# Performance work log

Measured on AMD Instinct MI355X. Metric: run time of the kernel, lower is better.

Reference implementation:

```python
import jax, jax.numpy as jnp
import numpy as np

TEMPERATURE = 0.07
BASE_TEMPERATURE = 0.07
EPI = 0.1
NUM_CLASSES = 100


def setup_inputs() -> dict:
    key = jax.random.key(0)
    k1, k2 = jax.random.split(key)
    bsz, n_views, d = 4096, 2, 256
    features = jax.random.normal(k1, (bsz, n_views, d), dtype=jnp.float32)
    # SupCon features are typically L2-normalized projections
    features = features / jnp.linalg.norm(features, axis=-1, keepdims=True)
    labels = jax.random.randint(k2, (bsz,), 0, NUM_CLASSES, dtype=jnp.int64)
    return {"features": features, "labels": labels}


def reference(features, labels):
    bsz, n_views, d = features.shape
    n = bsz * n_views
    # contrast_feature = cat(unbind(features, dim=1), dim=0): view-major ordering
    contrast = jnp.reshape(jnp.swapaxes(features, 0, 1), (n, d))  # [N, D]
    anchor = contrast  # contrast_mode == 'all'

    labels_t = jnp.tile(labels, n_views)  # [N], matches mask.repeat(anchor_count, contrast_count)
    mask_full = (labels_t[:, None] == labels_t[None, :]).astype(features.dtype)  # [N, N]

    # adversarial similarity: a_i . (c_j - epi * mask_ij * a_i) / T
    sq = jnp.sum(anchor * anchor, axis=1, keepdims=True)  # [N, 1]
    logits_raw = (jnp.matmul(anchor, contrast.T) - EPI * mask_full * sq) / TEMPERATURE

    logits_max = jax.lax.stop_gradient(jnp.max(logits_raw, axis=1, keepdims=True))
    logits = logits_raw - logits_max

    logits_mask = 1.0 - jnp.eye(n, dtype=features.dtype)  # mask out self-contrast
    mask = mask_full * logits_mask

    exp_logits = jnp.exp(logits) * logits_mask
    log_prob = logits - jnp.log(jnp.sum(exp_logits, axis=1, keepdims=True))
    mean_log_prob_pos = jnp.sum(mask * log_prob, axis=1) / jnp.sum(mask, axis=1)

    loss = -(TEMPERATURE / BASE_TEMPERATURE) * mean_log_prob_pos
    return jnp.mean(jnp.reshape(loss, (n_views, bsz)))
```

## Files before the change

### kernel.cpp

```cpp
#include <hip/hip_runtime.h>
#include <hip/hip_bf16.h>

#define NTOT 8192
#define NBSZ 4096
#define DDIM 256
#define NCHUNK 16
#define CHUNK_COLS 512
#define TILE_COLS 32
#define NT (CHUNK_COLS / TILE_COLS)
#define NCLASS 100

#define INV_T 14.285714285714286f
#define EPI_T 1.4285714285714286f
#define K1 20.609929155556076f
#define BIASS -2.0609929155556078f

typedef __attribute__((ext_vector_type(8))) __bf16 bf16x8;
typedef __attribute__((ext_vector_type(4))) float f32x4;

__device__ __forceinline__ unsigned short f2bf(float x) {
    union { float f; unsigned int u; } a; a.f = x;
    unsigned int r = a.u + 0x7fffu + ((a.u >> 16) & 1u);
    return (unsigned short)(r >> 16);
}

__global__ __launch_bounds__(256) void prep_kernel(const float* __restrict__ feat,
                                                   const int* __restrict__ labels,
                                                   unsigned short* __restrict__ Bg,
                                                   int* __restrict__ labT) {
    const int g = blockIdx.x * 256 + threadIdx.x;
    const int row = g >> 6, t = g & 63;
    const int v = row >> 12, b = row & (NBSZ - 1);
    const float* src = feat + (size_t)(b * 2 + v) * DDIM + t * 4;
    f32x4 val = *(const f32x4*)src;
    ushort4 o;
    o.x = f2bf(val[0]); o.y = f2bf(val[1]); o.z = f2bf(val[2]); o.w = f2bf(val[3]);
    *(ushort4*)(Bg + (size_t)row * DDIM + t * 4) = o;
    if (t == 0) labT[row] = labels[b];
}

__device__ __forceinline__ void stage_tile(const unsigned short* __restrict__ Bg,
                                           unsigned short* buf, int colBase, int tid) {
    #pragma unroll
    for (int it = 0; it < 4; ++it) {
        int c = it * 256 + tid;
        int brow = c >> 5, bc = c & 31;
        int sc = bc ^ (brow & 7);
        const unsigned short* src = Bg + (size_t)(colBase + brow) * DDIM + sc * 8;
        __builtin_amdgcn_global_load_lds(
            (const __attribute__((address_space(1))) void*)src,
            (__attribute__((address_space(3))) void*)(buf + (size_t)c * 8),
            16, 0, 0);
    }
}

__global__ __launch_bounds__(256, 2) void supcon_main(
    const unsigned short* __restrict__ Bg, const int* __restrict__ labT,
    float* __restrict__ pSe, float* __restrict__ pPd)
{
    __shared__ alignas(16) unsigned short btile[2][TILE_COLS * DDIM];
    __shared__ int labc_s[CHUNK_COLS];

    const int tid = threadIdx.x;
    const int wid = tid >> 6;
    const int lane = tid & 63;
    const int q = lane >> 4;
    const int r16 = lane & 15;

    const int rowBase = blockIdx.x * 256 + wid * 64;
    const int colChunk = blockIdx.y * CHUNK_COLS;

    labc_s[tid] = labT[colChunk + tid];
    labc_s[tid + 256] = labT[colChunk + 256 + tid];

    bf16x8 afr[4][8];
    #pragma unroll
    for (int m = 0; m < 4; ++m) {
        const unsigned short* ap = Bg + (size_t)(rowBase + m * 16 + r16) * DDIM + q * 8;
        #pragma unroll
        for (int ks = 0; ks < 8; ++ks)
            afr[m][ks] = *(const bf16x8*)(ap + ks * 32);
    }
    int labrow[4][4];
    #pragma unroll
    for (int m = 0; m < 4; ++m)
        #pragma unroll
        for (int r = 0; r < 4; ++r)
            labrow[m][r] = labT[rowBase + m * 16 + q * 4 + r];

    float se[4][4], pd[4][4];
    #pragma unroll
    for (int m = 0; m < 4; ++m)
        #pragma unroll
        for (int r = 0; r < 4; ++r) { se[m][r] = 0.f; pd[m][r] = 0.f; }

    stage_tile(Bg, btile[0], colChunk, tid);
    __syncthreads();

    for (int tile = 0; tile < NT; ++tile) {
        if (tile + 1 < NT)
            stage_tile(Bg, btile[(tile + 1) & 1], colChunk + (tile + 1) * TILE_COLS, tid);

        const unsigned short* bt = btile[tile & 1];
        f32x4 acc[4][2];
        #pragma unroll
        for (int m = 0; m < 4; ++m) { acc[m][0] = (f32x4)0.f; acc[m][1] = (f32x4)0.f; }

        __builtin_amdgcn_s_setprio(1);
        #pragma unroll
        for (int ks = 0; ks < 8; ++ks) {
            const int cx = (ks * 4 + q) ^ (r16 & 7);
            bf16x8 bq0 = *(const bf16x8*)(bt + r16 * DDIM + cx * 8);
            bf16x8 bq1 = *(const bf16x8*)(bt + (16 + r16) * DDIM + cx * 8);
            #pragma unroll
            for (int m = 0; m < 4; ++m) {
                acc[m][0] = __builtin_amdgcn_mfma_f32_16x16x32_bf16(afr[m][ks], bq0, acc[m][0], 0, 0, 0);
                acc[m][1] = __builtin_amdgcn_mfma_f32_16x16x32_bf16(afr[m][ks], bq1, acc[m][1], 0, 0, 0);
            }
        }
        __builtin_amdgcn_s_setprio(0);

        const int colBase = colChunk + tile * TILE_COLS;
        const int lc0 = labc_s[tile * TILE_COLS + r16];
        const int lc1 = labc_s[tile * TILE_COLS + 16 + r16];
        const bool diagT = ((unsigned)(colBase - rowBase)) < 64u;
        if (!diagT) {
            #pragma unroll
            for (int n = 0; n < 2; ++n) {
                const int lc = n ? lc1 : lc0;
                #pragma unroll
                for (int m = 0; m < 4; ++m)
                    #pragma unroll
                    for (int r = 0; r < 4; ++r) {
                        const bool same = (lc == labrow[m][r]);
                        float a = acc[m][n][r];
                        float t = fmaf(a, K1, same ? BIASS : 0.f);
                        se[m][r] += __builtin_amdgcn_exp2f(t);
                        pd[m][r] += same ? a : 0.f;
                    }
            }
        } else {
            #pragma unroll
            for (int n = 0; n < 2; ++n) {
                const int lc = n ? lc1 : lc0;
                const int gcol = colBase + n * 16 + r16;
                #pragma unroll
                for (int m = 0; m < 4; ++m)
                    #pragma unroll
                    for (int r = 0; r < 4; ++r) {
                        const int grow = rowBase + m * 16 + q * 4 + r;
                        const bool same = (lc == labrow[m][r]);
                        const bool keep = (grow != gcol);
                        float a = acc[m][n][r];
                        float t = fmaf(a, K1, same ? BIASS : 0.f);
                        float e = __builtin_amdgcn_exp2f(t);
                        se[m][r] += keep ? e : 0.f;
                        pd[m][r] += (same && keep) ? a : 0.f;
                    }
            }
        }
        __syncthreads();
    }

    #pragma unroll
    for (int mask = 1; mask <= 8; mask <<= 1)
        #pragma unroll
        for (int m = 0; m < 4; ++m)
            #pragma unroll
            for (int r = 0; r < 4; ++r) {
                se[m][r] += __shfl_xor(se[m][r], mask);
                pd[m][r] += __shfl_xor(pd[m][r], mask);
            }
    if (r16 == 0) {
        #pragma unroll
        for (int m = 0; m < 4; ++m) {
            const size_t o = (size_t)blockIdx.y * NTOT + rowBase + m * 16 + q * 4;
            f32x4 vs, vp;
            #pragma unroll
            for (int r = 0; r < 4; ++r) { vs[r] = se[m][r]; vp[r] = pd[m][r]; }
            *(f32x4*)(pSe + o) = vs;
            *(f32x4*)(pPd + o) = vp;
        }
    }
}

__global__ __launch_bounds__(256) void finalize_kernel(
    const int* __restrict__ labT, const float* __restrict__ pSe,
    const float* __restrict__ pPd, float* __restrict__ partial)
{
    __shared__ int hist[NCLASS];
    const int t = threadIdx.x;
    if (t < NCLASS) hist[t] = 0;
    __syncthreads();
    #pragma unroll
    for (int i = 0; i < NTOT / 256; ++i)
        atomicAdd(&hist[labT[i * 256 + t]], 1);
    __syncthreads();

    const int row = blockIdx.x * 256 + t;
    const int lab = labT[row];
    float se = 0.f, pd = 0.f;
    #pragma unroll
    for (int ch = 0; ch < NCHUNK; ++ch) {
        se += pSe[(size_t)ch * NTOT + row];
        pd += pPd[(size_t)ch * NTOT + row];
    }
    const float pc = (float)(hist[lab] - 1);
    float loss = EPI_T + __logf(se) - INV_T * pd / pc;

    #pragma unroll
    for (int mask = 1; mask < 64; mask <<= 1) loss += __shfl_xor(loss, mask);
    __shared__ float red[4];
    if ((t & 63) == 0) red[t >> 6] = loss;
    __syncthreads();
    if (t == 0) partial[blockIdx.x] = red[0] + red[1] + red[2] + red[3];
}

__global__ __launch_bounds__(64) void final_reduce(const float* __restrict__ partial,
                                                   float* __restrict__ out) {
    const int t = threadIdx.x;
    float s = (t < 32) ? partial[t] : 0.f;
    #pragma unroll
    for (int mask = 1; mask < 64; mask <<= 1) s += __shfl_xor(s, mask);
    if (t == 0) out[0] = s * (1.f / (float)NTOT);
}

extern "C" void kernel_launch(void* const* d_in, const int* in_sizes, int n_in,
                              void* d_out, int out_size, void* d_ws, size_t ws_size,
                              hipStream_t stream) {
    const float* feat = (const float*)d_in[0];
    const int* labels = (const int*)d_in[1];
    float* out = (float*)d_out;

    char* ws = (char*)d_ws;
    unsigned short* Bg = (unsigned short*)ws;
    int* labT = (int*)(ws + (4u << 20));
    float* pSe = (float*)(ws + (4u << 20) + (64u << 10));
    float* pPd = (float*)(ws + (4u << 20) + (576u << 10));
    float* partial = (float*)(ws + (4u << 20) + (1088u << 10));

    prep_kernel<<<2048, 256, 0, stream>>>(feat, labels, Bg, labT);
    dim3 grid(32, NCHUNK);
    supcon_main<<<grid, 256, 0, stream>>>(Bg, labT, pSe, pPd);
    finalize_kernel<<<32, 256, 0, stream>>>(labT, pSe, pPd, partial);
    final_reduce<<<1, 64, 0, stream>>>(partial, out);
}
```

Before: 63.97 us.

## Split columns into more chunks, accumulate via atomics, drop final reduce kernel

Halves the column chunk size so the main kernel launches twice as many blocks, and raises the launch-bounds occupancy hint from 2 to 4 blocks per SM. Per-chunk partial sums now go straight into per-row accumulators with float atomics, which the prep kernel zeroes first. The finalize kernel atomically adds into the output, so the separate final reduction launch goes away. The aim is better GPU fill and one less kernel launch, at the cost of atomic contention, order-dependent float sums, and register pressure from the higher occupancy target.

```diff
diff --git a/kernel.cpp b/kernel.cpp
--- a/kernel.cpp
+++ b/kernel.cpp
@@ -4,8 +4,8 @@
 #define NTOT 8192
 #define NBSZ 4096
 #define DDIM 256
-#define NCHUNK 16
-#define CHUNK_COLS 512
+#define NCHUNK 32
+#define CHUNK_COLS 256
 #define TILE_COLS 32
 #define NT (CHUNK_COLS / TILE_COLS)
 #define NCLASS 100
@@ -27,7 +27,10 @@
 __global__ __launch_bounds__(256) void prep_kernel(const float* __restrict__ feat,
                                                    const int* __restrict__ labels,
                                                    unsigned short* __restrict__ Bg,
-                                                   int* __restrict__ labT) {
+                                                   int* __restrict__ labT,
+                                                   float* __restrict__ pSe,
+                                                   float* __restrict__ pPd,
+                                                   float* __restrict__ out) {
     const int g = blockIdx.x * 256 + threadIdx.x;
     const int row = g >> 6, t = g & 63;
     const int v = row >> 12, b = row & (NBSZ - 1);
@@ -37,6 +40,9 @@
     o.x = f2bf(val[0]); o.y = f2bf(val[1]); o.z = f2bf(val[2]); o.w = f2bf(val[3]);
     *(ushort4*)(Bg + (size_t)row * DDIM + t * 4) = o;
     if (t == 0) labT[row] = labels[b];
+    if (g < NTOT) pSe[g] = 0.f;
+    else if (g < 2 * NTOT) pPd[g - NTOT] = 0.f;
+    if (g == 2 * NTOT) out[0] = 0.f;
 }
 
 __device__ __forceinline__ void stage_tile(const unsigned short* __restrict__ Bg,
@@ -54,7 +60,7 @@
     }
 }
 
-__global__ __launch_bounds__(256, 2) void supcon_main(
+__global__ __launch_bounds__(256, 4) void supcon_main(
     const unsigned short* __restrict__ Bg, const int* __restrict__ labT,
     float* __restrict__ pSe, float* __restrict__ pPd)
 {
@@ -71,7 +77,6 @@
     const int colChunk = blockIdx.y * CHUNK_COLS;
 
     labc_s[tid] = labT[colChunk + tid];
-    labc_s[tid + 256] = labT[colChunk + 256 + tid];
 
     bf16x8 afr[4][8];
     #pragma unroll
@@ -173,20 +178,19 @@
             }
     if (r16 == 0) {
         #pragma unroll
-        for (int m = 0; m < 4; ++m) {
-            const size_t o = (size_t)blockIdx.y * NTOT + rowBase + m * 16 + q * 4;
-            f32x4 vs, vp;
-            #pragma unroll
-            for (int r = 0; r < 4; ++r) { vs[r] = se[m][r]; vp[r] = pd[m][r]; }
-            *(f32x4*)(pSe + o) = vs;
-            *(f32x4*)(pPd + o) = vp;
-        }
+        for (int m = 0; m < 4; ++m)
+            #pragma unroll
+            for (int r = 0; r < 4; ++r) {
+                const int row = rowBase + m * 16 + q * 4 + r;
+                atomicAdd(&pSe[row], se[m][r]);
+                atomicAdd(&pPd[row], pd[m][r]);
+            }
     }
 }
 
 __global__ __launch_bounds__(256) void finalize_kernel(
     const int* __restrict__ labT, const float* __restrict__ pSe,
-    const float* __restrict__ pPd, float* __restrict__ partial)
+    const float* __restrict__ pPd, float* __restrict__ out)
 {
     __shared__ int hist[NCLASS];
     const int t = threadIdx.x;
@@ -199,12 +203,8 @@
 
     const int row = blockIdx.x * 256 + t;
     const int lab = labT[row];
-    float se = 0.f, pd = 0.f;
-    #pragma unroll
-    for (int ch = 0; ch < NCHUNK; ++ch) {
-        se += pSe[(size_t)ch * NTOT + row];
-        pd += pPd[(size_t)ch * NTOT + row];
-    }
+    const float se = pSe[row];
+    const float pd = pPd[row];
     const float pc = (float)(hist[lab] - 1);
     float loss = EPI_T + __logf(se) - INV_T * pd / pc;
 
@@ -213,16 +213,8 @@
     __shared__ float red[4];
     if ((t & 63) == 0) red[t >> 6] = loss;
     __syncthreads();
-    if (t == 0) partial[blockIdx.x] = red[0] + red[1] + red[2] + red[3];
-}
-
-__global__ __launch_bounds__(64) void final_reduce(const float* __restrict__ partial,
-                                                   float* __restrict__ out) {
-    const int t = threadIdx.x;
-    float s = (t < 32) ? partial[t] : 0.f;
-    #pragma unroll
-    for (int mask = 1; mask < 64; mask <<= 1) s += __shfl_xor(s, mask);
-    if (t == 0) out[0] = s * (1.f / (float)NTOT);
+    if (t == 0)
+        atomicAdd(out, (red[0] + red[1] + red[2] + red[3]) * (1.f / (float)NTOT));
 }
 
 extern "C" void kernel_launch(void* const* d_in, const int* in_sizes, int n_in,
@@ -236,12 +228,10 @@
     unsigned short* Bg = (unsigned short*)ws;
     int* labT = (int*)(ws + (4u << 20));
     float* pSe = (float*)(ws + (4u << 20) + (64u << 10));
-    float* pPd = (float*)(ws + (4u << 20) + (576u << 10));
-    float* partial = (float*)(ws + (4u << 20) + (1088u << 10));
-
-    prep_kernel<<<2048, 256, 0, stream>>>(feat, labels, Bg, labT);
+    float* pPd = (float*)(ws + (4u << 20) + (128u << 10));
+
+    prep_kernel<<<2048, 256, 0, stream>>>(feat, labels, Bg, labT, pSe, pPd, out);
     dim3 grid(32, NCHUNK);
     supcon_main<<<grid, 256, 0, stream>>>(Bg, labT, pSe, pPd);
-    finalize_kernel<<<32, 256, 0, stream>>>(labT, pSe, pPd, partial);
-    final_reduce<<<1, 64, 0, stream>>>(partial, out);
-}
+    finalize_kernel<<<32, 256, 0, stream>>>(labT, pSe, pPd, out);
+}
```

Result: slower. 229.0 us (+257.9%).

## Software-pipeline MFMA and epilogue across tiles and fold final reduce into atomics

Applied to the files above, without the earlier changes.

The main loop is restructured with two accumulator sets, so the MFMA for one tile is issued while the exp/mask epilogue of the previous tile runs. This lets matrix and vector work interleave instead of running back to back within each tile. The final_reduce launch is removed: prep zeroes the output and finalize blocks atomically add their scaled partials. The cost is higher register pressure from the doubled accumulators, and a float summation order that is no longer deterministic.

```diff
diff --git a/kernel.cpp b/kernel.cpp
--- a/kernel.cpp
+++ b/kernel.cpp
@@ -27,7 +27,8 @@
 __global__ __launch_bounds__(256) void prep_kernel(const float* __restrict__ feat,
                                                    const int* __restrict__ labels,
                                                    unsigned short* __restrict__ Bg,
-                                                   int* __restrict__ labT) {
+                                                   int* __restrict__ labT,
+                                                   float* __restrict__ out) {
     const int g = blockIdx.x * 256 + threadIdx.x;
     const int row = g >> 6, t = g & 63;
     const int v = row >> 12, b = row & (NBSZ - 1);
@@ -37,6 +38,7 @@
     o.x = f2bf(val[0]); o.y = f2bf(val[1]); o.z = f2bf(val[2]); o.w = f2bf(val[3]);
     *(ushort4*)(Bg + (size_t)row * DDIM + t * 4) = o;
     if (t == 0) labT[row] = labels[b];
+    if (g == 0) out[0] = 0.f;
 }
 
 __device__ __forceinline__ void stage_tile(const unsigned short* __restrict__ Bg,
@@ -54,6 +56,69 @@
     }
 }
 
+__device__ __forceinline__ void do_mfma(f32x4 (&acc)[4][2], const unsigned short* bt,
+                                        const bf16x8 (&afr)[4][8], int r16, int q) {
+    #pragma unroll
+    for (int m = 0; m < 4; ++m) { acc[m][0] = (f32x4)0.f; acc[m][1] = (f32x4)0.f; }
+    #pragma unroll
+    for (int ks = 0; ks < 8; ++ks) {
+        const int cx = (ks * 4 + q) ^ (r16 & 7);
+        bf16x8 bq0 = *(const bf16x8*)(bt + r16 * DDIM + cx * 8);
+        bf16x8 bq1 = *(const bf16x8*)(bt + (16 + r16) * DDIM + cx * 8);
+        #pragma unroll
+        for (int m = 0; m < 4; ++m) {
+            acc[m][0] = __builtin_amdgcn_mfma_f32_16x16x32_bf16(afr[m][ks], bq0, acc[m][0], 0, 0, 0);
+            acc[m][1] = __builtin_amdgcn_mfma_f32_16x16x32_bf16(afr[m][ks], bq1, acc[m][1], 0, 0, 0);
+        }
+    }
+}
+
+__device__ __forceinline__ void do_epi(const f32x4 (&acc)[4][2], int tile,
+                                       int colChunk, int rowBase,
+                                       const int* labc_s, const int (&labrow)[4][4],
+                                       float (&se)[4][4], float (&pd)[4][4],
+                                       int r16, int q) {
+    const int colBase = colChunk + tile * TILE_COLS;
+    const int lc0 = labc_s[tile * TILE_COLS + r16];
+    const int lc1 = labc_s[tile * TILE_COLS + 16 + r16];
+    const bool diagT = ((unsigned)(colBase - rowBase)) < 64u;
+    if (!diagT) {
+        #pragma unroll
+        for (int n = 0; n < 2; ++n) {
+            const int lc = n ? lc1 : lc0;
+            #pragma unroll
+            for (int m = 0; m < 4; ++m)
+                #pragma unroll
+                for (int r = 0; r < 4; ++r) {
+                    const bool same = (lc == labrow[m][r]);
+                    float a = acc[m][n][r];
+                    float t = fmaf(a, K1, same ? BIASS : 0.f);
+                    se[m][r] += __builtin_amdgcn_exp2f(t);
+                    pd[m][r] += same ? a : 0.f;
+                }
+        }
+    } else {
+        #pragma unroll
+        for (int n = 0; n < 2; ++n) {
+            const int lc = n ? lc1 : lc0;
+            const int gcol = colBase + n * 16 + r16;
+            #pragma unroll
+            for (int m = 0; m < 4; ++m)
+                #pragma unroll
+                for (int r = 0; r < 4; ++r) {
+                    const int grow = rowBase + m * 16 + q * 4 + r;
+                    const bool same = (lc == labrow[m][r]);
+                    const bool keep = (grow != gcol);
+                    float a = acc[m][n][r];
+                    float t = fmaf(a, K1, same ? BIASS : 0.f);
+                    float e = __builtin_amdgcn_exp2f(t);
+                    se[m][r] += keep ? e : 0.f;
+                    pd[m][r] += (same && keep) ? a : 0.f;
+                }
+        }
+    }
+}
+
 __global__ __launch_bounds__(256, 2) void supcon_main(
     const unsigned short* __restrict__ Bg, const int* __restrict__ labT,
     float* __restrict__ pSe, float* __restrict__ pPd)
@@ -71,7 +136,7 @@
     const int colChunk = blockIdx.y * CHUNK_COLS;
 
     labc_s[tid] = labT[colChunk + tid];
-    labc_s[tid + 256] = labT[colChunk + 256 + tid];
+    labc_s[256 + tid] = labT[colChunk + 256 + tid];
 
     bf16x8 afr[4][8];
     #pragma unroll
@@ -94,73 +159,28 @@
         #pragma unroll
         for (int r = 0; r < 4; ++r) { se[m][r] = 0.f; pd[m][r] = 0.f; }
 
+    f32x4 accA[4][2], accB[4][2];
+
     stage_tile(Bg, btile[0], colChunk, tid);
     __syncthreads();
-
-    for (int tile = 0; tile < NT; ++tile) {
-        if (tile + 1 < NT)
-            stage_tile(Bg, btile[(tile + 1) & 1], colChunk + (tile + 1) * TILE_COLS, tid);
-
-        const unsigned short* bt = btile[tile & 1];
-        f32x4 acc[4][2];
-        #pragma unroll
-        for (int m = 0; m < 4; ++m) { acc[m][0] = (f32x4)0.f; acc[m][1] = (f32x4)0.f; }
-
-        __builtin_amdgcn_s_setprio(1);
-        #pragma unroll
-        for (int ks = 0; ks < 8; ++ks) {
-            const int cx = (ks * 4 + q) ^ (r16 & 7);
-            bf16x8 bq0 = *(const bf16x8*)(bt + r16 * DDIM + cx * 8);
-            bf16x8 bq1 = *(const bf16x8*)(bt + (16 + r16) * DDIM + cx * 8);
-            #pragma unroll
-            for (int m = 0; m < 4; ++m) {
-                acc[m][0] = __builtin_amdgcn_mfma_f32_16x16x32_bf16(afr[m][ks], bq0, acc[m][0], 0, 0, 0);
-                acc[m][1] = __builtin_amdgcn_mfma_f32_16x16x32_bf16(afr[m][ks], bq1, acc[m][1], 0, 0, 0);
-            }
-        }
-        __builtin_amdgcn_s_setprio(0);
-
-        const int colBase = colChunk + tile * TILE_COLS;
-        const int lc0 = labc_s[tile * TILE_COLS + r16];
-        const int lc1 = labc_s[tile * TILE_COLS + 16 + r16];
-        const bool diagT = ((unsigned)(colBase - rowBase)) < 64u;
-        if (!diagT) {
-            #pragma unroll
-            for (int n = 0; n < 2; ++n) {
-                const int lc = n ? lc1 : lc0;
-                #pragma unroll
-                for (int m = 0; m < 4; ++m)
-                    #pragma unroll
-                    for (int r = 0; r < 4; ++r) {
-                        const bool same = (lc == labrow[m][r]);
-                        float a = acc[m][n][r];
-                        float t = fmaf(a, K1, same ? BIASS : 0.f);
-                        se[m][r] += __builtin_amdgcn_exp2f(t);
-                        pd[m][r] += same ? a : 0.f;
-                    }
-            }
-        } else {
-            #pragma unroll
-            for (int n = 0; n < 2; ++n) {
-                const int lc = n ? lc1 : lc0;
-                const int gcol = colBase + n * 16 + r16;
-                #pragma unroll
-                for (int m = 0; m < 4; ++m)
-                    #pragma unroll
-                    for (int r = 0; r < 4; ++r) {
-                        const int grow = rowBase + m * 16 + q * 4 + r;
-                        const bool same = (lc == labrow[m][r]);
-                        const bool keep = (grow != gcol);
-                        float a = acc[m][n][r];
-                        float t = fmaf(a, K1, same ? BIASS : 0.f);
-                        float e = __builtin_amdgcn_exp2f(t);
-                        se[m][r] += keep ? e : 0.f;
-                        pd[m][r] += (same && keep) ? a : 0.f;
-                    }
-            }
-        }
+    stage_tile(Bg, btile[1], colChunk + TILE_COLS, tid);
+    do_mfma(accA, btile[0], afr, r16, q);
+    __syncthreads();
+
+    for (int t = 1; t + 1 < NT; t += 2) {
+        stage_tile(Bg, btile[0], colChunk + (t + 1) * TILE_COLS, tid);
+        do_mfma(accB, btile[1], afr, r16, q);
+        do_epi(accA, t - 1, colChunk, rowBase, labc_s, labrow, se, pd, r16, q);
         __syncthreads();
-    }
+
+        stage_tile(Bg, btile[1], colChunk + (t + 2) * TILE_COLS, tid);
+        do_mfma(accA, btile[0], afr, r16, q);
+        do_epi(accB, t, colChunk, rowBase, labc_s, labrow, se, pd, r16, q);
+        __syncthreads();
+    }
+    do_mfma(accB, btile[1], afr, r16, q);
+    do_epi(accA, NT - 2, colChunk, rowBase, labc_s, labrow, se, pd, r16, q);
+    do_epi(accB, NT - 1, colChunk, rowBase, labc_s, labrow, se, pd, r16, q);
 
     #pragma unroll
     for (int mask = 1; mask <= 8; mask <<= 1)
@@ -186,7 +206,7 @@
 
 __global__ __launch_bounds__(256) void finalize_kernel(
     const int* __restrict__ labT, const float* __restrict__ pSe,
-    const float* __restrict__ pPd, float* __restrict__ partial)
+    const float* __restrict__ pPd, float* __restrict__ out)
 {
     __shared__ int hist[NCLASS];
     const int t = threadIdx.x;
@@ -199,30 +219,22 @@
 
     const int row = blockIdx.x * 256 + t;
     const int lab = labT[row];
-    float se = 0.f, pd = 0.f;
+    float se = 0.f, pdv = 0.f;
     #pragma unroll
     for (int ch = 0; ch < NCHUNK; ++ch) {
-        se += pSe[(size_t)ch * NTOT + row];
-        pd += pPd[(size_t)ch * NTOT + row];
+        se  += pSe[(size_t)ch * NTOT + row];
+        pdv += pPd[(size_t)ch * NTOT + row];
     }
     const float pc = (float)(hist[lab] - 1);
-    float loss = EPI_T + __logf(se) - INV_T * pd / pc;
+    float loss = EPI_T + __logf(se) - INV_T * pdv / pc;
 
     #pragma unroll
     for (int mask = 1; mask < 64; mask <<= 1) loss += __shfl_xor(loss, mask);
     __shared__ float red[4];
     if ((t & 63) == 0) red[t >> 6] = loss;
     __syncthreads();
-    if (t == 0) partial[blockIdx.x] = red[0] + red[1] + red[2] + red[3];
-}
-
-__global__ __launch_bounds__(64) void final_reduce(const float* __restrict__ partial,
-                                                   float* __restrict__ out) {
-    const int t = threadIdx.x;
-    float s = (t < 32) ? partial[t] : 0.f;
-    #pragma unroll
-    for (int mask = 1; mask < 64; mask <<= 1) s += __shfl_xor(s, mask);
-    if (t == 0) out[0] = s * (1.f / (float)NTOT);
+    if (t == 0)
+        atomicAdd(out, (red[0] + red[1] + red[2] + red[3]) * (1.f / (float)NTOT));
 }
 
 extern "C" void kernel_launch(void* const* d_in, const int* in_sizes, int n_in,
@@ -237,11 +249,9 @@
     int* labT = (int*)(ws + (4u << 20));
     float* pSe = (float*)(ws + (4u << 20) + (64u << 10));
     float* pPd = (float*)(ws + (4u << 20) + (576u << 10));
-    float* partial = (float*)(ws + (4u << 20) + (1088u << 10));
-
-    prep_kernel<<<2048, 256, 0, stream>>>(feat, labels, Bg, labT);
+
+    prep_kernel<<<2048, 256, 0, stream>>>(feat, labels, Bg, labT, out);
     dim3 grid(32, NCHUNK);
     supcon_main<<<grid, 256, 0, stream>>>(Bg, labT, pSe, pPd);
-    finalize_kernel<<<32, 256, 0, stream>>>(labT, pSe, pPd, partial);
-    final_reduce<<<1, 64, 0, stream>>>(partial, out);
-}
+    finalize_kernel<<<32, 256, 0, stream>>>(labT, pSe, pPd, out);
+}
```

Result: slower. 120.3 us (+88.1%).

## Split same-class correction into per-class kernel, simplify main exp-sum epilogue

Applied to the files above, without the earlier changes.

The main N×N kernel now sums plain exp(a·K1) over all columns with no label compares, diagonal handling or positive-dot accumulation. A new per-class kernel computes the same-class Gram blocks. From these it derives the self term, the same-class exp sum (corrected by the factor 1−e^{-bias}) and the positive dot sums, which the finalize kernel subtracts algebraically. The final_reduce launch is replaced by an atomicAdd into the output, which prep_kernel zeroes. The cost is an extra launch and a CAP=192 per-class list limit that silently truncates larger classes, and the subtraction of large terms may lose precision.

```diff
diff --git a/kernel.cpp b/kernel.cpp
--- a/kernel.cpp
+++ b/kernel.cpp
@@ -9,11 +9,12 @@
 #define TILE_COLS 32
 #define NT (CHUNK_COLS / TILE_COLS)
 #define NCLASS 100
+#define CAP 192
 
 #define INV_T 14.285714285714286f
 #define EPI_T 1.4285714285714286f
 #define K1 20.609929155556076f
-#define BIASS -2.0609929155556078f
+#define ONE_M_2B 0.7603489635148818f
 
 typedef __attribute__((ext_vector_type(8))) __bf16 bf16x8;
 typedef __attribute__((ext_vector_type(4))) float f32x4;
@@ -27,7 +28,8 @@
 __global__ __launch_bounds__(256) void prep_kernel(const float* __restrict__ feat,
                                                    const int* __restrict__ labels,
                                                    unsigned short* __restrict__ Bg,
-                                                   int* __restrict__ labT) {
+                                                   int* __restrict__ labT,
+                                                   float* __restrict__ out) {
     const int g = blockIdx.x * 256 + threadIdx.x;
     const int row = g >> 6, t = g & 63;
     const int v = row >> 12, b = row & (NBSZ - 1);
@@ -37,6 +39,93 @@
     o.x = f2bf(val[0]); o.y = f2bf(val[1]); o.z = f2bf(val[2]); o.w = f2bf(val[3]);
     *(ushort4*)(Bg + (size_t)row * DDIM + t * 4) = o;
     if (t == 0) labT[row] = labels[b];
+    if (g == 0) out[0] = 0.f;
+}
+
+__global__ __launch_bounds__(256) void classcorr_kernel(
+    const unsigned short* __restrict__ Bg, const int* __restrict__ labT,
+    float* __restrict__ C1, float* __restrict__ Pd, float* __restrict__ SelfE)
+{
+    const int c = blockIdx.x;
+    const int t = threadIdx.x;
+    const int wid = t >> 6, lane = t & 63;
+    const int q = lane >> 4, r16 = lane & 15;
+    __shared__ unsigned short list[CAP];
+    __shared__ int wsum[4];
+
+    int cntLoc = 0;
+    #pragma unroll
+    for (int k = 0; k < 32; ++k) cntLoc += (labT[t + 256 * k] == c) ? 1 : 0;
+    int incl = cntLoc;
+    #pragma unroll
+    for (int d = 1; d < 64; d <<= 1) {
+        int up = __shfl_up(incl, d);
+        if (lane >= d) incl += up;
+    }
+    if (lane == 63) wsum[wid] = incl;
+    __syncthreads();
+    int off = incl - cntLoc;
+    for (int w = 0; w < wid; ++w) off += wsum[w];
+    const int cnt = wsum[0] + wsum[1] + wsum[2] + wsum[3];
+    for (int k = 0; k < 32; ++k) {
+        int row = t + 256 * k;
+        if (labT[row] == c && off < CAP) list[off++] = (unsigned short)row;
+    }
+    __syncthreads();
+
+    const int ntile = (cnt + 15) >> 4;
+    for (int ti = wid; ti < ntile; ti += 4) {
+        const int ilocB = ti * 16 + q * 4;
+        const int ia = ti * 16 + r16;
+        const int rowA = list[(ia < cnt) ? ia : 0];
+        const unsigned short* ap = Bg + (size_t)rowA * DDIM + q * 8;
+        bf16x8 af[8];
+        #pragma unroll
+        for (int ks = 0; ks < 8; ++ks) af[ks] = *(const bf16x8*)(ap + ks * 32);
+
+        float c1a[4] = {0.f, 0.f, 0.f, 0.f};
+        float pda[4] = {0.f, 0.f, 0.f, 0.f};
+        for (int tj = 0; tj < ntile; ++tj) {
+            const int jslot = tj * 16 + r16;
+            const int rowB = list[(jslot < cnt) ? jslot : 0];
+            const unsigned short* bp = Bg + (size_t)rowB * DDIM + q * 8;
+            bf16x8 bf[8];
+            #pragma unroll
+            for (int ks = 0; ks < 8; ++ks) bf[ks] = *(const bf16x8*)(bp + ks * 32);
+            f32x4 acc = (f32x4)0.f;
+            #pragma unroll
+            for (int ks = 0; ks < 8; ++ks)
+                acc = __builtin_amdgcn_mfma_f32_16x16x32_bf16(af[ks], bf[ks], acc, 0, 0, 0);
+            #pragma unroll
+            for (int r = 0; r < 4; ++r) {
+                const int islot = ilocB + r;
+                const bool valid = (islot < cnt) && (jslot < cnt);
+                const bool self = (islot == jslot);
+                float a = acc[r];
+                float e = __builtin_amdgcn_exp2f(a * K1);
+                if (valid && self) SelfE[list[islot]] = e;
+                c1a[r] += (valid && !self) ? e : 0.f;
+                pda[r] += (valid && !self) ? a : 0.f;
+            }
+        }
+        #pragma unroll
+        for (int mask = 1; mask <= 8; mask <<= 1)
+            #pragma unroll
+            for (int r = 0; r < 4; ++r) {
+                c1a[r] += __shfl_xor(c1a[r], mask);
+                pda[r] += __shfl_xor(pda[r], mask);
+            }
+        if (r16 == 0) {
+            #pragma unroll
+            for (int r = 0; r < 4; ++r) {
+                const int islot = ilocB + r;
+                if (islot < cnt) {
+                    C1[list[islot]] = c1a[r];
+                    Pd[list[islot]] = pda[r];
+                }
+            }
+        }
+    }
 }
 
 __device__ __forceinline__ void stage_tile(const unsigned short* __restrict__ Bg,
@@ -55,11 +144,9 @@
 }
 
 __global__ __launch_bounds__(256, 2) void supcon_main(
-    const unsigned short* __restrict__ Bg, const int* __restrict__ labT,
-    float* __restrict__ pSe, float* __restrict__ pPd)
+    const unsigned short* __restrict__ Bg, float* __restrict__ pSe)
 {
     __shared__ alignas(16) unsigned short btile[2][TILE_COLS * DDIM];
-    __shared__ int labc_s[CHUNK_COLS];
 
     const int tid = threadIdx.x;
     const int wid = tid >> 6;
@@ -70,9 +157,6 @@
     const int rowBase = blockIdx.x * 256 + wid * 64;
     const int colChunk = blockIdx.y * CHUNK_COLS;
 
-    labc_s[tid] = labT[colChunk + tid];
-    labc_s[tid + 256] = labT[colChunk + 256 + tid];
-
     bf16x8 afr[4][8];
     #pragma unroll
     for (int m = 0; m < 4; ++m) {
@@ -81,18 +165,12 @@
         for (int ks = 0; ks < 8; ++ks)
             afr[m][ks] = *(const bf16x8*)(ap + ks * 32);
     }
-    int labrow[4][4];
+
+    float se[4][4];
     #pragma unroll
     for (int m = 0; m < 4; ++m)
         #pragma unroll
-        for (int r = 0; r < 4; ++r)
-            labrow[m][r] = labT[rowBase + m * 16 + q * 4 + r];
-
-    float se[4][4], pd[4][4];
-    #pragma unroll
-    for (int m = 0; m < 4; ++m)
-        #pragma unroll
-        for (int r = 0; r < 4; ++r) { se[m][r] = 0.f; pd[m][r] = 0.f; }
+        for (int r = 0; r < 4; ++r) se[m][r] = 0.f;
 
     stage_tile(Bg, btile[0], colChunk, tid);
     __syncthreads();
@@ -120,45 +198,14 @@
         }
         __builtin_amdgcn_s_setprio(0);
 
-        const int colBase = colChunk + tile * TILE_COLS;
-        const int lc0 = labc_s[tile * TILE_COLS + r16];
-        const int lc1 = labc_s[tile * TILE_COLS + 16 + r16];
-        const bool diagT = ((unsigned)(colBase - rowBase)) < 64u;
-        if (!diagT) {
-            #pragma unroll
-            for (int n = 0; n < 2; ++n) {
-                const int lc = n ? lc1 : lc0;
+        #pragma unroll
+        for (int n = 0; n < 2; ++n)
+            #pragma unroll
+            for (int m = 0; m < 4; ++m)
                 #pragma unroll
-                for (int m = 0; m < 4; ++m)
-                    #pragma unroll
-                    for (int r = 0; r < 4; ++r) {
-                        const bool same = (lc == labrow[m][r]);
-                        float a = acc[m][n][r];
-                        float t = fmaf(a, K1, same ? BIASS : 0.f);
-                        se[m][r] += __builtin_amdgcn_exp2f(t);
-                        pd[m][r] += same ? a : 0.f;
-                    }
-            }
-        } else {
-            #pragma unroll
-            for (int n = 0; n < 2; ++n) {
-                const int lc = n ? lc1 : lc0;
-                const int gcol = colBase + n * 16 + r16;
-                #pragma unroll
-                for (int m = 0; m < 4; ++m)
-                    #pragma unroll
-                    for (int r = 0; r < 4; ++r) {
-                        const int grow = rowBase + m * 16 + q * 4 + r;
-                        const bool same = (lc == labrow[m][r]);
-                        const bool keep = (grow != gcol);
-                        float a = acc[m][n][r];
-                        float t = fmaf(a, K1, same ? BIASS : 0.f);
-                        float e = __builtin_amdgcn_exp2f(t);
-                        se[m][r] += keep ? e : 0.f;
-                        pd[m][r] += (same && keep) ? a : 0.f;
-                    }
-            }
-        }
+                for (int r = 0; r < 4; ++r)
+                    se[m][r] += __builtin_amdgcn_exp2f(acc[m][n][r] * K1);
+
         __syncthreads();
     }
 
@@ -167,26 +214,24 @@
         #pragma unroll
         for (int m = 0; m < 4; ++m)
             #pragma unroll
-            for (int r = 0; r < 4; ++r) {
+            for (int r = 0; r < 4; ++r)
                 se[m][r] += __shfl_xor(se[m][r], mask);
-                pd[m][r] += __shfl_xor(pd[m][r], mask);
-            }
     if (r16 == 0) {
         #pragma unroll
         for (int m = 0; m < 4; ++m) {
             const size_t o = (size_t)blockIdx.y * NTOT + rowBase + m * 16 + q * 4;
-            f32x4 vs, vp;
-            #pragma unroll
-            for (int r = 0; r < 4; ++r) { vs[r] = se[m][r]; vp[r] = pd[m][r]; }
+            f32x4 vs;
+            #pragma unroll
+            for (int r = 0; r < 4; ++r) vs[r] = se[m][r];
             *(f32x4*)(pSe + o) = vs;
-            *(f32x4*)(pPd + o) = vp;
         }
     }
 }
 
 __global__ __launch_bounds__(256) void finalize_kernel(
     const int* __restrict__ labT, const float* __restrict__ pSe,
-    const float* __restrict__ pPd, float* __restrict__ partial)
+    const float* __restrict__ C1, const float* __restrict__ Pd,
+    const float* __restrict__ SelfE, float* __restrict__ out)
 {
     __shared__ int hist[NCLASS];
     const int t = threadIdx.x;
@@ -199,30 +244,21 @@
 
     const int row = blockIdx.x * 256 + t;
     const int lab = labT[row];
-    float se = 0.f, pd = 0.f;
-    #pragma unroll
-    for (int ch = 0; ch < NCHUNK; ++ch) {
-        se += pSe[(size_t)ch * NTOT + row];
-        pd += pPd[(size_t)ch * NTOT + row];
-    }
+    float se = 0.f;
+    #pragma unroll
+    for (int ch = 0; ch < NCHUNK; ++ch) se += pSe[(size_t)ch * NTOT + row];
+    se = se - SelfE[row] - ONE_M_2B * C1[row];
+
     const float pc = (float)(hist[lab] - 1);
-    float loss = EPI_T + __logf(se) - INV_T * pd / pc;
+    float loss = EPI_T + __logf(se) - INV_T * Pd[row] / pc;
 
     #pragma unroll
     for (int mask = 1; mask < 64; mask <<= 1) loss += __shfl_xor(loss, mask);
     __shared__ float red[4];
     if ((t & 63) == 0) red[t >> 6] = loss;
     __syncthreads();
-    if (t == 0) partial[blockIdx.x] = red[0] + red[1] + red[2] + red[3];
-}
-
-__global__ __launch_bounds__(64) void final_reduce(const float* __restrict__ partial,
-                                                   float* __restrict__ out) {
-    const int t = threadIdx.x;
-    float s = (t < 32) ? partial[t] : 0.f;
-    #pragma unroll
-    for (int mask = 1; mask < 64; mask <<= 1) s += __shfl_xor(s, mask);
-    if (t == 0) out[0] = s * (1.f / (float)NTOT);
+    if (t == 0)
+        atomicAdd(out, (red[0] + red[1] + red[2] + red[3]) * (1.f / (float)NTOT));
 }
 
 extern "C" void kernel_launch(void* const* d_in, const int* in_sizes, int n_in,
@@ -236,12 +272,13 @@
     unsigned short* Bg = (unsigned short*)ws;
     int* labT = (int*)(ws + (4u << 20));
     float* pSe = (float*)(ws + (4u << 20) + (64u << 10));
-    float* pPd = (float*)(ws + (4u << 20) + (576u << 10));
-    float* partial = (float*)(ws + (4u << 20) + (1088u << 10));
-
-    prep_kernel<<<2048, 256, 0, stream>>>(feat, labels, Bg, labT);
+    float* C1v = (float*)(ws + (4u << 20) + (576u << 10));
+    float* Pdv = (float*)(ws + (4u << 20) + (640u << 10));
+    float* SEv = (float*)(ws + (4u << 20) + (704u << 10));
+
+    prep_kernel<<<2048, 256, 0, stream>>>(feat, labels, Bg, labT, out);
+    classcorr_kernel<<<NCLASS, 256, 0, stream>>>(Bg, labT, C1v, Pdv, SEv);
     dim3 grid(32, NCHUNK);
-    supcon_main<<<grid, 256, 0, stream>>>(Bg, labT, pSe, pPd);
-    finalize_kernel<<<32, 256, 0, stream>>>(labT, pSe, pPd, partial);
-    final_reduce<<<1, 64, 0, stream>>>(partial, out);
-}
+    supcon_main<<<grid, 256, 0, stream>>>(Bg, pSe);
+    finalize_kernel<<<32, 256, 0, stream>>>(labT, pSe, C1v, Pdv, SEv, out);
+}
```

New measurement: 78.23 us. 1.22x slower.
